# Kernel optimization log

Measured on AMD Instinct MI355X. Metric: run time of the kernel, lower is better.

## Reference

```python
import jax, jax.numpy as jnp
import numpy as np

B, T, I, H, O = 1024, 512, 64, 256, 1


def setup_inputs() -> dict:
    key = jax.random.key(0)
    ks = jax.random.split(key, 7)
    s_ih = 1.0 / np.sqrt(H)
    return {
        "input_seq": jax.random.normal(ks[0], (B, T, I), dtype=jnp.float32),
        "W_ih": jax.random.uniform(ks[1], (4 * H, I), jnp.float32, -s_ih, s_ih),
        "W_hh": jax.random.uniform(ks[2], (4 * H, H), jnp.float32, -s_ih, s_ih),
        "b_ih": jax.random.uniform(ks[3], (4 * H,), jnp.float32, -s_ih, s_ih),
        "b_hh": jax.random.uniform(ks[4], (4 * H,), jnp.float32, -s_ih, s_ih),
        "W_out": jax.random.uniform(ks[5], (O, H), jnp.float32, -s_ih, s_ih),
        "b_out": jax.random.uniform(ks[6], (O,), jnp.float32, -s_ih, s_ih),
    }


def reference(input_seq, W_ih, W_hh, b_ih, b_hh, W_out, b_out):
    batch = input_seq.shape[0]
    hid = W_hh.shape[1]
    h0 = jnp.zeros((batch, hid), dtype=input_seq.dtype)
    c0 = jnp.zeros((batch, hid), dtype=input_seq.dtype)

    def step(carry, x_t):
        h, c = carry
        # PyTorch LSTMCell gate order: i, f, g, o
        gates = x_t @ W_ih.T + b_ih + h @ W_hh.T + b_hh  # [B, 4H]
        i, f, g, o = jnp.split(gates, 4, axis=-1)
        i = jax.nn.sigmoid(i)
        f = jax.nn.sigmoid(f)
        g = jnp.tanh(g)
        o = jax.nn.sigmoid(o)
        c_new = f * c + i * g
        h_new = o * jnp.tanh(c_new)
        return (h_new, c_new), None

    xs = jnp.swapaxes(input_seq, 0, 1)  # [T, B, I]
    (h_last, _), _ = jax.lax.scan(step, (h0, c0), xs)
    return h_last @ W_out.T + b_out  # [B, O]
```

## Files before the change

### kernel.cpp

```cpp
#include <hip/hip_runtime.h>
#include <hip/hip_bf16.h>


typedef float f32x4 __attribute__((ext_vector_type(4)));
typedef short s16x8 __attribute__((ext_vector_type(8)));

#define BB 1024
#define TT 512
#define II 64
#define HH 256
#define GG 1024

__device__ __forceinline__ ushort f2bf(float f) {
  unsigned u = __builtin_bit_cast(unsigned, f);
  u = (u + 0x7FFFu + ((u >> 16) & 1u)) >> 16;
  return (ushort)u;
}

__device__ __forceinline__ float sigm(float x) {
  return 1.0f / (1.0f + __expf(-x));
}
__device__ __forceinline__ float tanh_s(float x) {
  float e = __expf(-2.0f * fabsf(x));
  float t = (1.0f - e) / (1.0f + e);
  return copysignf(t, x);
}

__global__ void cvt_weights(const float* __restrict__ wih,
                            const float* __restrict__ whh,
                            ushort* __restrict__ ws) {
  int i = blockIdx.x * 256 + threadIdx.x;
  if (i < GG * II) {
    ws[i] = f2bf(wih[i]);
  } else {
    int j = i - GG * II;
    if (j < GG * HH) ws[GG * II + j] = f2bf(whh[j]);
  }
}

template <bool BF>
__device__ __forceinline__ s16x8 load_bfrag(const void* base, int off) {
  if constexpr (BF) {
    return *(const s16x8*)((const ushort*)base + off);
  } else {
    const float* p = (const float*)base + off;
    f32x4 a = *(const f32x4*)p;
    f32x4 b = *(const f32x4*)(p + 4);
    s16x8 r;
    r[0] = (short)f2bf(a[0]); r[1] = (short)f2bf(a[1]);
    r[2] = (short)f2bf(a[2]); r[3] = (short)f2bf(a[3]);
    r[4] = (short)f2bf(b[0]); r[5] = (short)f2bf(b[1]);
    r[6] = (short)f2bf(b[2]); r[7] = (short)f2bf(b[3]);
    return r;
  }
}

template <bool WSBF>
__global__ __launch_bounds__(512, 2) void lstm_main(
    const float* __restrict__ x,
    const float* __restrict__ wih_f,
    const float* __restrict__ whh_f,
    const float* __restrict__ b_ih,
    const float* __restrict__ b_hh,
    const float* __restrict__ w_out,
    const float* __restrict__ b_out,
    const ushort* __restrict__ wsb,
    float* __restrict__ out)
{
  __shared__ ushort h_lds[16 * 256];
  __shared__ float hf[16][256];

  const int tid  = threadIdx.x;
  const int wv   = tid >> 6;
  const int l    = tid & 63;
  const int lrow = l & 15;
  const int lk8  = (l >> 4) << 3;
  const int crow = (l >> 4) << 2;
  const int ccol = l & 15;
  const int b0 = blockIdx.x << 4;
  const int jw = wv << 5;

  {
    s16x8 z = {};
    *(s16x8*)&h_lds[tid * 8] = z;
  }

  const void* wih_base = WSBF ? (const void*)wsb : (const void*)wih_f;
  const void* whh_base = WSBF ? (const void*)(wsb + GG * II) : (const void*)whh_f;

  s16x8 wih_frag[4][2][2];
#pragma unroll
  for (int g = 0; g < 4; ++g)
#pragma unroll
    for (int nt = 0; nt < 2; ++nt)
#pragma unroll
      for (int kt = 0; kt < 2; ++kt) {
        int jrow = g * 256 + jw + nt * 16 + lrow;
        wih_frag[g][nt][kt] = load_bfrag<WSBF>(wih_base, jrow * II + kt * 32 + lk8);
      }

  float bs[4][2];
#pragma unroll
  for (int g = 0; g < 4; ++g)
#pragma unroll
    for (int nt = 0; nt < 2; ++nt) {
      int c = g * 256 + jw + nt * 16 + ccol;
      bs[g][nt] = b_ih[c] + b_hh[c];
    }

  float cst[2][4] = {};

  __syncthreads();

  for (int t = 0; t < TT; ++t) {
    s16x8 xf[2];
    {
      const float* xp = x + ((size_t)(b0 + lrow) * TT + t) * II + lk8;
#pragma unroll
      for (int kt = 0; kt < 2; ++kt) {
        f32x4 a = *(const f32x4*)(xp + kt * 32);
        f32x4 b = *(const f32x4*)(xp + kt * 32 + 4);
        s16x8 r;
        r[0] = (short)f2bf(a[0]); r[1] = (short)f2bf(a[1]);
        r[2] = (short)f2bf(a[2]); r[3] = (short)f2bf(a[3]);
        r[4] = (short)f2bf(b[0]); r[5] = (short)f2bf(b[1]);
        r[6] = (short)f2bf(b[2]); r[7] = (short)f2bf(b[3]);
        xf[kt] = r;
      }
    }
    s16x8 hfr[8];
#pragma unroll
    for (int kt = 0; kt < 8; ++kt) {
      int byte = lrow * 512 + (kt * 32 + lk8) * 2;
      byte ^= (lrow & 7) << 4;
      hfr[kt] = *(const s16x8*)((const char*)h_lds + byte);
    }

    f32x4 acc[4][2];
#pragma unroll
    for (int g = 0; g < 4; ++g)
#pragma unroll
      for (int nt = 0; nt < 2; ++nt) {
        f32x4 a;
        a[0] = a[1] = a[2] = a[3] = bs[g][nt];
        s16x8 bw[8];
        int jrow = g * 256 + jw + nt * 16 + lrow;
#pragma unroll
        for (int kt = 0; kt < 8; ++kt)
          bw[kt] = load_bfrag<WSBF>(whh_base, jrow * HH + kt * 32 + lk8);
        a = __builtin_amdgcn_mfma_f32_16x16x32_bf16(xf[0], wih_frag[g][nt][0], a, 0, 0, 0);
        a = __builtin_amdgcn_mfma_f32_16x16x32_bf16(xf[1], wih_frag[g][nt][1], a, 0, 0, 0);
#pragma unroll
        for (int kt = 0; kt < 8; ++kt)
          a = __builtin_amdgcn_mfma_f32_16x16x32_bf16(hfr[kt], bw[kt], a, 0, 0, 0);
        acc[g][nt] = a;
      }

    __syncthreads();

#pragma unroll
    for (int nt = 0; nt < 2; ++nt)
#pragma unroll
      for (int r = 0; r < 4; ++r) {
        float gi = sigm(acc[0][nt][r]);
        float gf = sigm(acc[1][nt][r]);
        float gg = tanh_s(acc[2][nt][r]);
        float go = sigm(acc[3][nt][r]);
        float cn = gf * cst[nt][r] + gi * gg;
        cst[nt][r] = cn;
        float hn = go * tanh_s(cn);
        int row = crow + r;
        int col = jw + nt * 16 + ccol;
        int byte = (row * 512 + col * 2) ^ ((row & 7) << 4);
        *(ushort*)((char*)h_lds + byte) = f2bf(hn);
        if (t == TT - 1) hf[row][col] = hn;
      }

    __syncthreads();
  }

#pragma unroll
  for (int rr = 0; rr < 2; ++rr) {
    int row = wv * 2 + rr;
    float s = 0.f;
#pragma unroll
    for (int m = 0; m < 4; ++m)
      s += hf[row][l + 64 * m] * w_out[l + 64 * m];
#pragma unroll
    for (int off = 32; off >= 1; off >>= 1)
      s += __shfl_xor(s, off);
    if (l == 0) out[b0 + row] = s + b_out[0];
  }
}

extern "C" void kernel_launch(void* const* d_in, const int* in_sizes, int n_in,
                              void* d_out, int out_size, void* d_ws, size_t ws_size,
                              hipStream_t stream) {
  const float* x     = (const float*)d_in[0];
  const float* wih   = (const float*)d_in[1];
  const float* whh   = (const float*)d_in[2];
  const float* b_ih  = (const float*)d_in[3];
  const float* b_hh  = (const float*)d_in[4];
  const float* w_out = (const float*)d_in[5];
  const float* b_out = (const float*)d_in[6];
  float* out = (float*)d_out;

  const size_t ws_needed = (size_t)(GG * II + GG * HH) * sizeof(ushort);
  if (ws_size >= ws_needed) {
    ushort* wsb = (ushort*)d_ws;
    int n = GG * II + GG * HH;
    cvt_weights<<<(n + 255) / 256, 256, 0, stream>>>(wih, whh, wsb);
    lstm_main<true><<<BB / 16, 512, 0, stream>>>(x, wih, whh, b_ih, b_hh, w_out,
                                                 b_out, wsb, out);
  } else {
    lstm_main<false><<<BB / 16, 512, 0, stream>>>(x, wih, whh, b_ih, b_hh, w_out,
                                                  b_out, nullptr, out);
  }
}
```

Before: 7.132 ms.

## Keep recurrent weights in registers with 16-wave blocks and double-buffered hidden state

```diff
diff --git a/kernel.cpp b/kernel.cpp
--- a/kernel.cpp
+++ b/kernel.cpp
@@ -5,11 +5,9 @@
 typedef float f32x4 __attribute__((ext_vector_type(4)));
 typedef short s16x8 __attribute__((ext_vector_type(8)));
 
-#define BB 1024
 #define TT 512
 #define II 64
 #define HH 256
-#define GG 1024
 
 __device__ __forceinline__ ushort f2bf(float f) {
   unsigned u = __builtin_bit_cast(unsigned, f);
@@ -26,37 +24,18 @@
   return copysignf(t, x);
 }
 
-__global__ void cvt_weights(const float* __restrict__ wih,
-                            const float* __restrict__ whh,
-                            ushort* __restrict__ ws) {
-  int i = blockIdx.x * 256 + threadIdx.x;
-  if (i < GG * II) {
-    ws[i] = f2bf(wih[i]);
-  } else {
-    int j = i - GG * II;
-    if (j < GG * HH) ws[GG * II + j] = f2bf(whh[j]);
-  }
+__device__ __forceinline__ s16x8 pack_bf8(const float* p) {
+  f32x4 a = *(const f32x4*)p;
+  f32x4 b = *(const f32x4*)(p + 4);
+  s16x8 r;
+  r[0] = (short)f2bf(a[0]); r[1] = (short)f2bf(a[1]);
+  r[2] = (short)f2bf(a[2]); r[3] = (short)f2bf(a[3]);
+  r[4] = (short)f2bf(b[0]); r[5] = (short)f2bf(b[1]);
+  r[6] = (short)f2bf(b[2]); r[7] = (short)f2bf(b[3]);
+  return r;
 }
 
-template <bool BF>
-__device__ __forceinline__ s16x8 load_bfrag(const void* base, int off) {
-  if constexpr (BF) {
-    return *(const s16x8*)((const ushort*)base + off);
-  } else {
-    const float* p = (const float*)base + off;
-    f32x4 a = *(const f32x4*)p;
-    f32x4 b = *(const f32x4*)(p + 4);
-    s16x8 r;
-    r[0] = (short)f2bf(a[0]); r[1] = (short)f2bf(a[1]);
-    r[2] = (short)f2bf(a[2]); r[3] = (short)f2bf(a[3]);
-    r[4] = (short)f2bf(b[0]); r[5] = (short)f2bf(b[1]);
-    r[6] = (short)f2bf(b[2]); r[7] = (short)f2bf(b[3]);
-    return r;
-  }
-}
-
-template <bool WSBF>
-__global__ __launch_bounds__(512, 2) void lstm_main(
+__global__ __launch_bounds__(1024, 4) void lstm_one(
     const float* __restrict__ x,
     const float* __restrict__ wih_f,
     const float* __restrict__ whh_f,
@@ -64,10 +43,9 @@
     const float* __restrict__ b_hh,
     const float* __restrict__ w_out,
     const float* __restrict__ b_out,
-    const ushort* __restrict__ wsb,
     float* __restrict__ out)
 {
-  __shared__ ushort h_lds[16 * 256];
+  __shared__ ushort h_lds[2][16 * 256];
   __shared__ float hf[16][256];
 
   const int tid  = threadIdx.x;
@@ -77,119 +55,112 @@
   const int lk8  = (l >> 4) << 3;
   const int crow = (l >> 4) << 2;
   const int ccol = l & 15;
-  const int b0 = blockIdx.x << 4;
-  const int jw = wv << 5;
+  const int b0   = blockIdx.x << 4;
+  const int col0 = wv << 4;
 
-  {
-    s16x8 z = {};
-    *(s16x8*)&h_lds[tid * 8] = z;
+  s16x8 whh[4][8];
+  s16x8 wih[4][2];
+  float bs[4];
+#pragma unroll
+  for (int g = 0; g < 4; ++g) {
+    const int wrow = g * 256 + col0 + lrow;
+#pragma unroll
+    for (int kf = 0; kf < 8; ++kf)
+      whh[g][kf] = pack_bf8(whh_f + wrow * HH + kf * 32 + lk8);
+#pragma unroll
+    for (int kf = 0; kf < 2; ++kf)
+      wih[g][kf] = pack_bf8(wih_f + wrow * II + kf * 32 + lk8);
+    const int c = g * 256 + col0 + ccol;
+    bs[g] = b_ih[c] + b_hh[c];
   }
 
-  const void* wih_base = WSBF ? (const void*)wsb : (const void*)wih_f;
-  const void* whh_base = WSBF ? (const void*)(wsb + GG * II) : (const void*)whh_f;
+  float cst[4] = {0.f, 0.f, 0.f, 0.f};
 
-  s16x8 wih_frag[4][2][2];
+  f32x4 accn[4];
+  {
+    const float* xp = x + (size_t)(b0 + lrow) * TT * II + lk8;
+    s16x8 x0 = pack_bf8(xp);
+    s16x8 x1 = pack_bf8(xp + 32);
 #pragma unroll
-  for (int g = 0; g < 4; ++g)
+    for (int g = 0; g < 4; ++g) {
+      f32x4 a;
+      a[0] = a[1] = a[2] = a[3] = bs[g];
+      a = __builtin_amdgcn_mfma_f32_16x16x32_bf16(x0, wih[g][0], a, 0, 0, 0);
+      a = __builtin_amdgcn_mfma_f32_16x16x32_bf16(x1, wih[g][1], a, 0, 0, 0);
+      accn[g] = a;
+    }
+  }
+
+  for (int t = 0; t < TT; ++t) {
+    s16x8 hfr[8];
+    if (t > 0) {
 #pragma unroll
-    for (int nt = 0; nt < 2; ++nt)
-#pragma unroll
-      for (int kt = 0; kt < 2; ++kt) {
-        int jrow = g * 256 + jw + nt * 16 + lrow;
-        wih_frag[g][nt][kt] = load_bfrag<WSBF>(wih_base, jrow * II + kt * 32 + lk8);
+      for (int kf = 0; kf < 8; ++kf) {
+        int byte = (lrow * 512 + (kf * 32 + lk8) * 2) ^ ((lrow & 7) << 4);
+        hfr[kf] = *(const s16x8*)((const char*)h_lds[t & 1] + byte);
       }
-
-  float bs[4][2];
-#pragma unroll
-  for (int g = 0; g < 4; ++g)
-#pragma unroll
-    for (int nt = 0; nt < 2; ++nt) {
-      int c = g * 256 + jw + nt * 16 + ccol;
-      bs[g][nt] = b_ih[c] + b_hh[c];
     }
 
-  float cst[2][4] = {};
+    s16x8 xn0, xn1;
+    if (t < TT - 1) {
+      const float* xp = x + ((size_t)(b0 + lrow) * TT + (t + 1)) * II + lk8;
+      xn0 = pack_bf8(xp);
+      xn1 = pack_bf8(xp + 32);
+    }
 
-  __syncthreads();
+    f32x4 acc[4];
+#pragma unroll
+    for (int g = 0; g < 4; ++g) {
+      f32x4 a = accn[g];
+      if (t > 0) {
+#pragma unroll
+        for (int kf = 0; kf < 8; ++kf)
+          a = __builtin_amdgcn_mfma_f32_16x16x32_bf16(hfr[kf], whh[g][kf], a,
+                                                      0, 0, 0);
+      }
+      acc[g] = a;
+    }
 
-  for (int t = 0; t < TT; ++t) {
-    s16x8 xf[2];
-    {
-      const float* xp = x + ((size_t)(b0 + lrow) * TT + t) * II + lk8;
+    if (t < TT - 1) {
 #pragma unroll
-      for (int kt = 0; kt < 2; ++kt) {
-        f32x4 a = *(const f32x4*)(xp + kt * 32);
-        f32x4 b = *(const f32x4*)(xp + kt * 32 + 4);
-        s16x8 r;
-        r[0] = (short)f2bf(a[0]); r[1] = (short)f2bf(a[1]);
-        r[2] = (short)f2bf(a[2]); r[3] = (short)f2bf(a[3]);
-        r[4] = (short)f2bf(b[0]); r[5] = (short)f2bf(b[1]);
-        r[6] = (short)f2bf(b[2]); r[7] = (short)f2bf(b[3]);
-        xf[kt] = r;
+      for (int g = 0; g < 4; ++g) {
+        f32x4 a;
+        a[0] = a[1] = a[2] = a[3] = bs[g];
+        a = __builtin_amdgcn_mfma_f32_16x16x32_bf16(xn0, wih[g][0], a, 0, 0, 0);
+        a = __builtin_amdgcn_mfma_f32_16x16x32_bf16(xn1, wih[g][1], a, 0, 0, 0);
+        accn[g] = a;
       }
     }
-    s16x8 hfr[8];
-#pragma unroll
-    for (int kt = 0; kt < 8; ++kt) {
-      int byte = lrow * 512 + (kt * 32 + lk8) * 2;
-      byte ^= (lrow & 7) << 4;
-      hfr[kt] = *(const s16x8*)((const char*)h_lds + byte);
-    }
-
-    f32x4 acc[4][2];
-#pragma unroll
-    for (int g = 0; g < 4; ++g)
-#pragma unroll
-      for (int nt = 0; nt < 2; ++nt) {
-        f32x4 a;
-        a[0] = a[1] = a[2] = a[3] = bs[g][nt];
-        s16x8 bw[8];
-        int jrow = g * 256 + jw + nt * 16 + lrow;
-#pragma unroll
-        for (int kt = 0; kt < 8; ++kt)
-          bw[kt] = load_bfrag<WSBF>(whh_base, jrow * HH + kt * 32 + lk8);
-        a = __builtin_amdgcn_mfma_f32_16x16x32_bf16(xf[0], wih_frag[g][nt][0], a, 0, 0, 0);
-        a = __builtin_amdgcn_mfma_f32_16x16x32_bf16(xf[1], wih_frag[g][nt][1], a, 0, 0, 0);
-#pragma unroll
-        for (int kt = 0; kt < 8; ++kt)
-          a = __builtin_amdgcn_mfma_f32_16x16x32_bf16(hfr[kt], bw[kt], a, 0, 0, 0);
-        acc[g][nt] = a;
-      }
-
-    __syncthreads();
 
 #pragma unroll
-    for (int nt = 0; nt < 2; ++nt)
-#pragma unroll
-      for (int r = 0; r < 4; ++r) {
-        float gi = sigm(acc[0][nt][r]);
-        float gf = sigm(acc[1][nt][r]);
-        float gg = tanh_s(acc[2][nt][r]);
-        float go = sigm(acc[3][nt][r]);
-        float cn = gf * cst[nt][r] + gi * gg;
-        cst[nt][r] = cn;
-        float hn = go * tanh_s(cn);
-        int row = crow + r;
-        int col = jw + nt * 16 + ccol;
+    for (int r = 0; r < 4; ++r) {
+      float gi = sigm(acc[0][r]);
+      float gf = sigm(acc[1][r]);
+      float gg = tanh_s(acc[2][r]);
+      float go = sigm(acc[3][r]);
+      float cn = gf * cst[r] + gi * gg;
+      cst[r] = cn;
+      float hn = go * tanh_s(cn);
+      int row = crow + r;
+      int col = col0 + ccol;
+      if (t == TT - 1) {
+        hf[row][col] = hn;
+      } else {
         int byte = (row * 512 + col * 2) ^ ((row & 7) << 4);
-        *(ushort*)((char*)h_lds + byte) = f2bf(hn);
-        if (t == TT - 1) hf[row][col] = hn;
+        *(ushort*)((char*)h_lds[(t + 1) & 1] + byte) = f2bf(hn);
       }
+    }
 
     __syncthreads();
   }
 
+  {
+    float s = hf[wv][l] * w_out[l] + hf[wv][l + 64] * w_out[l + 64] +
+              hf[wv][l + 128] * w_out[l + 128] +
+              hf[wv][l + 192] * w_out[l + 192];
 #pragma unroll
-  for (int rr = 0; rr < 2; ++rr) {
-    int row = wv * 2 + rr;
-    float s = 0.f;
-#pragma unroll
-    for (int m = 0; m < 4; ++m)
-      s += hf[row][l + 64 * m] * w_out[l + 64 * m];
-#pragma unroll
-    for (int off = 32; off >= 1; off >>= 1)
-      s += __shfl_xor(s, off);
-    if (l == 0) out[b0 + row] = s + b_out[0];
+    for (int off = 32; off >= 1; off >>= 1) s += __shfl_xor(s, off);
+    if (l == 0) out[b0 + wv] = s + b_out[0];
   }
 }
 
@@ -205,15 +176,5 @@
   const float* b_out = (const float*)d_in[6];
   float* out = (float*)d_out;
 
-  const size_t ws_needed = (size_t)(GG * II + GG * HH) * sizeof(ushort);
-  if (ws_size >= ws_needed) {
-    ushort* wsb = (ushort*)d_ws;
-    int n = GG * II + GG * HH;
-    cvt_weights<<<(n + 255) / 256, 256, 0, stream>>>(wih, whh, wsb);
-    lstm_main<true><<<BB / 16, 512, 0, stream>>>(x, wih, whh, b_ih, b_hh, w_out,
-                                                 b_out, wsb, out);
-  } else {
-    lstm_main<false><<<BB / 16, 512, 0, stream>>>(x, wih, whh, b_ih, b_hh, w_out,
-                                                  b_out, nullptr, out);
-  }
+  lstm_one<<<64, 1024, 0, stream>>>(x, wih, whh, b_ih, b_hh, w_out, b_out, out);
 }
```

New measurement: 8.790 ms. 1.23x slower.

## Double-buffer weight fragment loads and prefetch next-step input in LSTM loop

Applied to the files above, without the earlier changes.

```diff
diff --git a/kernel.cpp b/kernel.cpp
--- a/kernel.cpp
+++ b/kernel.cpp
@@ -5,7 +5,6 @@
 typedef float f32x4 __attribute__((ext_vector_type(4)));
 typedef short s16x8 __attribute__((ext_vector_type(8)));
 
-#define BB 1024
 #define TT 512
 #define II 64
 #define HH 256
@@ -24,6 +23,17 @@
   float e = __expf(-2.0f * fabsf(x));
   float t = (1.0f - e) / (1.0f + e);
   return copysignf(t, x);
+}
+
+__device__ __forceinline__ s16x8 pack_bf8(const float* p) {
+  f32x4 a = *(const f32x4*)p;
+  f32x4 b = *(const f32x4*)(p + 4);
+  s16x8 r;
+  r[0] = (short)f2bf(a[0]); r[1] = (short)f2bf(a[1]);
+  r[2] = (short)f2bf(a[2]); r[3] = (short)f2bf(a[3]);
+  r[4] = (short)f2bf(b[0]); r[5] = (short)f2bf(b[1]);
+  r[6] = (short)f2bf(b[2]); r[7] = (short)f2bf(b[3]);
+  return r;
 }
 
 __global__ void cvt_weights(const float* __restrict__ wih,
@@ -38,25 +48,17 @@
   }
 }
 
-template <bool BF>
-__device__ __forceinline__ s16x8 load_bfrag(const void* base, int off) {
-  if constexpr (BF) {
+template <bool WSBF>
+__device__ __forceinline__ s16x8 load_frag(const void* base, int off) {
+  if constexpr (WSBF) {
     return *(const s16x8*)((const ushort*)base + off);
   } else {
-    const float* p = (const float*)base + off;
-    f32x4 a = *(const f32x4*)p;
-    f32x4 b = *(const f32x4*)(p + 4);
-    s16x8 r;
-    r[0] = (short)f2bf(a[0]); r[1] = (short)f2bf(a[1]);
-    r[2] = (short)f2bf(a[2]); r[3] = (short)f2bf(a[3]);
-    r[4] = (short)f2bf(b[0]); r[5] = (short)f2bf(b[1]);
-    r[6] = (short)f2bf(b[2]); r[7] = (short)f2bf(b[3]);
-    return r;
+    return pack_bf8((const float*)base + off);
   }
 }
 
 template <bool WSBF>
-__global__ __launch_bounds__(512, 2) void lstm_main(
+__global__ __launch_bounds__(512, 2) void lstm_stream(
     const float* __restrict__ x,
     const float* __restrict__ wih_f,
     const float* __restrict__ whh_f,
@@ -88,17 +90,6 @@
   const void* wih_base = WSBF ? (const void*)wsb : (const void*)wih_f;
   const void* whh_base = WSBF ? (const void*)(wsb + GG * II) : (const void*)whh_f;
 
-  s16x8 wih_frag[4][2][2];
-#pragma unroll
-  for (int g = 0; g < 4; ++g)
-#pragma unroll
-    for (int nt = 0; nt < 2; ++nt)
-#pragma unroll
-      for (int kt = 0; kt < 2; ++kt) {
-        int jrow = g * 256 + jw + nt * 16 + lrow;
-        wih_frag[g][nt][kt] = load_bfrag<WSBF>(wih_base, jrow * II + kt * 32 + lk8);
-      }
-
   float bs[4][2];
 #pragma unroll
   for (int g = 0; g < 4; ++g)
@@ -110,51 +101,58 @@
 
   float cst[2][4] = {};
 
+  s16x8 xf0, xf1;
+  {
+    const float* xp = x + (size_t)(b0 + lrow) * TT * II + lk8;
+    xf0 = pack_bf8(xp);
+    xf1 = pack_bf8(xp + 32);
+  }
+
   __syncthreads();
 
+#define ROWOF(ii) (((ii) >> 1) * 256 + jw + ((ii) & 1) * 16 + lrow)
+#define STAGE(ii, buf)                                                        \
+  {                                                                           \
+    const int row_ = ROWOF(ii);                                               \
+    _Pragma("unroll") for (int kf = 0; kf < 8; ++kf)                          \
+        stg[buf][kf] = load_frag<WSBF>(whh_base, row_ * HH + kf * 32 + lk8);  \
+    _Pragma("unroll") for (int kt = 0; kt < 2; ++kt)                          \
+        stg[buf][8 + kt] = load_frag<WSBF>(wih_base, row_ * II + kt * 32 + lk8); \
+  }
+
   for (int t = 0; t < TT; ++t) {
-    s16x8 xf[2];
-    {
-      const float* xp = x + ((size_t)(b0 + lrow) * TT + t) * II + lk8;
-#pragma unroll
-      for (int kt = 0; kt < 2; ++kt) {
-        f32x4 a = *(const f32x4*)(xp + kt * 32);
-        f32x4 b = *(const f32x4*)(xp + kt * 32 + 4);
-        s16x8 r;
-        r[0] = (short)f2bf(a[0]); r[1] = (short)f2bf(a[1]);
-        r[2] = (short)f2bf(a[2]); r[3] = (short)f2bf(a[3]);
-        r[4] = (short)f2bf(b[0]); r[5] = (short)f2bf(b[1]);
-        r[6] = (short)f2bf(b[2]); r[7] = (short)f2bf(b[3]);
-        xf[kt] = r;
-      }
-    }
     s16x8 hfr[8];
 #pragma unroll
-    for (int kt = 0; kt < 8; ++kt) {
-      int byte = lrow * 512 + (kt * 32 + lk8) * 2;
-      byte ^= (lrow & 7) << 4;
-      hfr[kt] = *(const s16x8*)((const char*)h_lds + byte);
+    for (int kf = 0; kf < 8; ++kf) {
+      int byte = (lrow * 512 + (kf * 32 + lk8) * 2) ^ ((lrow & 7) << 4);
+      hfr[kf] = *(const s16x8*)((const char*)h_lds + byte);
+    }
+
+    s16x8 xn0, xn1;
+    if (t < TT - 1) {
+      const float* xp = x + ((size_t)(b0 + lrow) * TT + (t + 1)) * II + lk8;
+      xn0 = pack_bf8(xp);
+      xn1 = pack_bf8(xp + 32);
     }
 
     f32x4 acc[4][2];
-#pragma unroll
-    for (int g = 0; g < 4; ++g)
-#pragma unroll
-      for (int nt = 0; nt < 2; ++nt) {
-        f32x4 a;
-        a[0] = a[1] = a[2] = a[3] = bs[g][nt];
-        s16x8 bw[8];
-        int jrow = g * 256 + jw + nt * 16 + lrow;
-#pragma unroll
-        for (int kt = 0; kt < 8; ++kt)
-          bw[kt] = load_bfrag<WSBF>(whh_base, jrow * HH + kt * 32 + lk8);
-        a = __builtin_amdgcn_mfma_f32_16x16x32_bf16(xf[0], wih_frag[g][nt][0], a, 0, 0, 0);
-        a = __builtin_amdgcn_mfma_f32_16x16x32_bf16(xf[1], wih_frag[g][nt][1], a, 0, 0, 0);
-#pragma unroll
-        for (int kt = 0; kt < 8; ++kt)
-          a = __builtin_amdgcn_mfma_f32_16x16x32_bf16(hfr[kt], bw[kt], a, 0, 0, 0);
-        acc[g][nt] = a;
-      }
+    s16x8 stg[2][10];
+    STAGE(0, 0)
+    STAGE(1, 1)
+#pragma unroll
+    for (int ii = 0; ii < 8; ++ii) {
+      const int g = ii >> 1, nt = ii & 1, buf = ii & 1;
+      f32x4 a;
+      a[0] = a[1] = a[2] = a[3] = bs[g][nt];
+      a = __builtin_amdgcn_mfma_f32_16x16x32_bf16(xf0, stg[buf][8], a, 0, 0, 0);
+      a = __builtin_amdgcn_mfma_f32_16x16x32_bf16(xf1, stg[buf][9], a, 0, 0, 0);
+#pragma unroll
+      for (int kf = 0; kf < 8; ++kf)
+        a = __builtin_amdgcn_mfma_f32_16x16x32_bf16(hfr[kf], stg[buf][kf], a,
+                                                    0, 0, 0);
+      acc[g][nt] = a;
+      if (ii < 6) STAGE(ii + 2, buf)
+    }
 
     __syncthreads();
 
@@ -176,6 +174,8 @@
         if (t == TT - 1) hf[row][col] = hn;
       }
 
+    xf0 = xn0;
+    xf1 = xn1;
     __syncthreads();
   }
 
@@ -191,6 +191,8 @@
       s += __shfl_xor(s, off);
     if (l == 0) out[b0 + row] = s + b_out[0];
   }
+#undef STAGE
+#undef ROWOF
 }
 
 extern "C" void kernel_launch(void* const* d_in, const int* in_sizes, int n_in,
@@ -210,10 +212,10 @@
     ushort* wsb = (ushort*)d_ws;
     int n = GG * II + GG * HH;
     cvt_weights<<<(n + 255) / 256, 256, 0, stream>>>(wih, whh, wsb);
-    lstm_main<true><<<BB / 16, 512, 0, stream>>>(x, wih, whh, b_ih, b_hh, w_out,
-                                                 b_out, wsb, out);
+    lstm_stream<true><<<64, 512, 0, stream>>>(x, wih, whh, b_ih, b_hh, w_out,
+                                              b_out, wsb, out);
   } else {
-    lstm_main<false><<<BB / 16, 512, 0, stream>>>(x, wih, whh, b_ih, b_hh, w_out,
-                                                  b_out, nullptr, out);
-  }
-}
+    lstm_stream<false><<<64, 512, 0, stream>>>(x, wih, whh, b_ih, b_hh, w_out,
+                                               b_out, nullptr, out);
+  }
+}
```

After: 8.305 ms. +16.4%, slower.
